# Kernel optimization log

Hardware: AMD Instinct MI355X
Metric: run time of the kernel (lower is better)

The kernel has to match this reference:

```python
import jax, jax.numpy as jnp
import numpy as np

NUM_WIRES = 14
N_LAYERS = 4
BATCH = 128


def _rx_mat(theta):
    # PennyLane RX(t) = [[cos(t/2), -i sin(t/2)], [-i sin(t/2), cos(t/2)]]
    c = jnp.cos(theta / 2).astype(jnp.complex64)
    s = jnp.sin(theta / 2).astype(jnp.complex64)
    row0 = jnp.stack([c, -1j * s], axis=-1)
    row1 = jnp.stack([-1j * s, c], axis=-1)
    return jnp.stack([row0, row1], axis=-2)  # (..., 2, 2)


def _rz_mat(theta):
    # PennyLane RZ(t) = diag(exp(-it/2), exp(it/2))
    e0 = jnp.exp(-1j * theta.astype(jnp.complex64) / 2)
    e1 = jnp.exp(1j * theta.astype(jnp.complex64) / 2)
    z = jnp.zeros_like(e0)
    row0 = jnp.stack([e0, z], axis=-1)
    row1 = jnp.stack([z, e1], axis=-1)
    return jnp.stack([row0, row1], axis=-2)


def _apply_1q(psi, gate, wire):
    # psi: (B, 2, 2, ..., 2); gate: (2,2) shared or (B,2,2) per-sample
    axis = wire + 1
    psi = jnp.moveaxis(psi, axis, -1)
    if gate.ndim == 2:
        psi = psi @ gate.T
    else:
        psi = jnp.einsum('b...j,bij->b...i', psi, gate)
    return jnp.moveaxis(psi, -1, axis)


def _apply_cnot(psi, ctrl, tgt):
    ac, at = ctrl + 1, tgt + 1
    psi0 = jnp.take(psi, 0, axis=ac)
    psi1 = jnp.take(psi, 1, axis=ac)
    at_adj = at - (1 if at > ac else 0)  # target axis shifts after removing ctrl axis
    psi1 = jnp.flip(psi1, axis=at_adj)   # X on target when ctrl=1
    return jnp.stack([psi0, psi1], axis=ac)


def _circuit(x, weights):
    # x: (B, n) real angles; weights: (L, n, 2)
    B = x.shape[0]
    n = NUM_WIRES
    psi = jnp.zeros((B,) + (2,) * n, jnp.complex64)
    psi = psi.at[(slice(None),) + (0,) * n].set(1.0)  # |0...0>
    # data encoding: per-sample RX gates
    for i in range(n):
        psi = _apply_1q(psi, _rx_mat(x[:, i]), i)
    # variational ansatz
    for l in range(N_LAYERS):
        for i in range(n):
            psi = _apply_1q(psi, _rx_mat(weights[l, i, 0]), i)
            psi = _apply_1q(psi, _rz_mat(weights[l, i, 1]), i)
        for i in range(n - 1):
            psi = _apply_cnot(psi, i, i + 1)
        psi = _apply_cnot(psi, n - 1, 0)
    # <Z_i> for every wire
    p = jnp.abs(psi) ** 2  # (B, 2, ..., 2) real
    zs = []
    for i in range(n):
        other = tuple(a for a in range(1, n + 1) if a != i + 1)
        m = jnp.sum(p, axis=other)  # (B, 2)
        zs.append(m[:, 0] - m[:, 1])
    return jnp.stack(zs, axis=-1)  # (B, n)


def setup_inputs() -> dict:
    key = jax.random.key(0)
    k1, k2, k3, k4 = jax.random.split(key, 4)
    states = jax.random.normal(k1, (BATCH, 2 ** NUM_WIRES), dtype=jnp.float32)
    weights = jax.random.normal(k2, (N_LAYERS, NUM_WIRES, 2), dtype=jnp.float32)
    lim = 1.0 / np.sqrt(NUM_WIRES)
    head_w = jax.random.uniform(k3, (1, NUM_WIRES), jnp.float32, -lim, lim)
    head_b = jax.random.uniform(k4, (1,), jnp.float32, -lim, lim)
    return {"states": states, "weights": weights, "head_w": head_w, "head_b": head_b}


def reference(states, weights, head_w, head_b):
    features = jnp.abs(states)[:, :NUM_WIRES]        # (B, n)
    qfeatures = _circuit(features, weights)          # (B, n)
    out = (qfeatures @ head_w.T + head_b)[:, 0]      # (B,)
    return out
```

## Files before the change

kernel.cpp:

```cpp
#include <hip/hip_runtime.h>
#include <math.h>

#define NW 14
#define NSTATE 16384
#define HALF 8192
#define NL 4
#define BATCH 128
#define TPB 1024
#define SHB1 (84 * 1024)
#define SHB2 ((NSTATE + 3 * TPB) * (int)sizeof(float2))


#define B12_ 0x3FFFu
#define B13_ 0x1FFFu

#define WAVE_FENCE() __builtin_amdgcn_wave_barrier()

__device__ __forceinline__ unsigned sxmap(unsigned v) {
    unsigned t = v;
    t ^= t >> 1; t ^= t >> 2; t ^= t >> 4; t ^= t >> 8;
    return (t & 0x0FFFu) | ((t & 1u) << 13);
}

__device__ __forceinline__ float2 cmul(float2 u, float2 v) {
    return make_float2(u.x * v.x - u.y * v.y, u.x * v.y + u.y * v.x);
}

__device__ __forceinline__ float4 fused_coef(const float* weights,
                                             const float* states,
                                             int b, int l, int w) {
    float t1 = weights[(l * NW + w) * 2 + 0];
    float t2 = weights[(l * NW + w) * 2 + 1];
    if (l == 0) t1 += fabsf(states[(size_t)b * NSTATE + w]);
    float s, c, sz, cz;
    sincosf(0.5f * t1, &s, &c);
    sincosf(0.5f * t2, &sz, &cz);
    return make_float4(c * cz, -c * sz, -s * sz, -s * cz);
}

template<int N, int M>
__device__ __forceinline__ void gateN(float2* r, float4 g, unsigned s3) {
    const float f = (s3 & (unsigned)M) ? -1.0f : 1.0f;
    g.y *= f;
    g.z *= f;
#pragma unroll
    for (int k = 0; k < N; ++k) {
        if ((k & M) == 0) {
            const float x0 = r[k].x,   y0 = r[k].y;
            const float x1 = r[k|M].x, y1 = r[k|M].y;
            r[k].x   =  g.x*x0 - g.y*y0 + g.z*x1 - g.w*y1;
            r[k].y   =  g.x*y0 + g.y*x0 + g.z*y1 + g.w*x1;
            r[k|M].x = -g.z*x0 - g.w*y0 + g.x*x1 + g.y*y1;
            r[k|M].y = -g.z*y0 + g.w*x0 + g.x*y1 - g.y*x1;
        }
    }
}

template<int J0, int S3SH, int S3MSK>
__device__ __forceinline__ void pass3h(float2* psi, const float4* gc,
                                       unsigned t) {
    const float4 gA = gc[13 - (J0 + 0)];
    const float4 gB = gc[13 - (J0 + 1)];
    const float4 gC = gc[13 - (J0 + 2)];
    const unsigned s3   = (t >> S3SH) & (unsigned)S3MSK;
    const unsigned low  = t & ((1u << J0) - 1u);
    const unsigned high = (t >> J0) << (J0 + 3);
    float2 r[8];
#pragma unroll
    for (int k = 0; k < 8; ++k)
        r[k] = psi[low | (((unsigned)k ^ s3) << J0) | high];
    gateN<8,1>(r, gA, s3);
    gateN<8,2>(r, gB, s3);
    gateN<8,4>(r, gC, s3);
#pragma unroll
    for (int k = 0; k < 8; ++k)
        psi[low | (((unsigned)k ^ s3) << J0) | high] = r[k];
}

template<int J0, bool SWZ>
__device__ __forceinline__ void pass4f(float2* psi, const float4* gc,
                                       unsigned t) {
    const float4 gA = gc[13 - (J0 + 0)];
    const float4 gB = gc[13 - (J0 + 1)];
    const float4 gC = gc[13 - (J0 + 2)];
    const float4 gD = gc[13 - (J0 + 3)];
    const unsigned s    = SWZ ? (t & 15u) : 0u;
    const unsigned low  = t & ((1u << J0) - 1u);
    const unsigned high = (t >> J0) << (J0 + 4);
    float2 r[16];
#pragma unroll
    for (int k = 0; k < 16; ++k)
        r[k] = psi[low | (((unsigned)k ^ s) << J0) | high];
    gateN<16,1>(r, gA, s);
    gateN<16,2>(r, gB, s);
    gateN<16,4>(r, gC, s);
    gateN<16,8>(r, gD, s);
#pragma unroll
    for (int k = 0; k < 16; ++k)
        psi[low | (((unsigned)k ^ s) << J0) | high] = r[k];
}

__device__ __forceinline__ void passE(float2* psi, float2* spare,
                                      const float4* gc4, int l, unsigned t) {
    const float4 g1 = gc4[l*NW + 1];
    const float4 g0 = gc4[l*NW + 0];

    unsigned v = t;
    v ^= v >> 1; v ^= v >> 2; v ^= v >> 4; v ^= v >> 8;
    const unsigned Rinv0 = (v & 0x0FFFu) | ((v & 1u) << 13);

    float2 c0[4];
#pragma unroll
    for (int k = 0; k < 4; ++k) c0[k] = psi[t | ((unsigned)k << 12)];
    gateN<4,1>(c0, g1, 0u);
    gateN<4,2>(c0, g0, 0u);
    spare[3*t+0] = c0[1];
    spare[3*t+1] = c0[2];
    spare[3*t+2] = c0[3];
    const float2 keep = c0[0];

    float2 r[12];
#pragma unroll
    for (int m = 1; m < 4; ++m) {
        const unsigned base = t | ((unsigned)m << 10);
#pragma unroll
        for (int k = 0; k < 4; ++k)
            r[(m-1)*4 + k] = psi[base | ((unsigned)k << 12)];
    }
#pragma unroll
    for (int m = 0; m < 3; ++m) {
        gateN<4,1>(r + 4*m, g1, 0u);
        gateN<4,2>(r + 4*m, g0, 0u);
    }

    __syncthreads();

#pragma unroll
    for (int m = 1; m < 4; ++m) {
        const unsigned Rb = Rinv0 ^ ((m & 1) ? 0x27FFu : 0u)
                                  ^ ((m & 2) ? 0x2FFFu : 0u);
#pragma unroll
        for (int k = 0; k < 4; ++k) {
            const unsigned CK = ((k & 1) ? B12_ : 0u) ^ ((k & 2) ? B13_ : 0u);
            psi[Rb ^ CK] = r[(m-1)*4 + k];
        }
    }
    psi[Rinv0]           = keep;
    psi[Rinv0 ^ B12_]    = spare[3*t+0];
    psi[Rinv0 ^ B13_]    = spare[3*t+1];
    psi[Rinv0 ^ 0x2000u] = spare[3*t+2];
}

__device__ __forceinline__ void exit_scatter(const float2* psi,
                                             float2* __restrict__ dst,
                                             float4 g1, unsigned q,
                                             unsigned tid) {
#pragma unroll
    for (int m = 0; m < 4; ++m) {
        const unsigned jc = tid + (unsigned)m * TPB;
        const float2 x0 = psi[jc];
        const float2 x1 = psi[jc | 0x1000u];
        float2 A0, A1;
        A0.x =  g1.x*x0.x - g1.y*x0.y + g1.z*x1.x - g1.w*x1.y;
        A0.y =  g1.x*x0.y + g1.y*x0.x + g1.z*x1.y + g1.w*x1.x;
        A1.x = -g1.z*x0.x - g1.w*x0.y + g1.x*x1.x + g1.y*x1.y;
        A1.y = -g1.z*x0.y + g1.w*x0.x + g1.x*x1.y - g1.y*x1.x;
        const unsigned d0 = sxmap(jc) ^ (q ? 0x1FFFu : 0u);
        dst[d0]           = A0;
        dst[d0 ^ 0x3FFFu] = A1;
    }
}

__global__ __launch_bounds__(TPB) void k_layer1(
    const float* __restrict__ states, const float* __restrict__ weights,
    float2* __restrict__ Sout)
{
    extern __shared__ float2 psi[];
    __shared__ float2 vfac[NW][2];
    __shared__ float2 T1[128];
    __shared__ float2 T2[128];
    __shared__ float4 gc[NW];
    const unsigned gid = blockIdx.x, q = gid >> 7, b = gid & 127u;
    const unsigned tid = threadIdx.x;

    if (tid < NW) {
        float4 g = fused_coef(weights, states, (int)b, 0, (int)tid);
        vfac[tid][0] = make_float2(g.x, g.y);
        vfac[tid][1] = make_float2(-g.z, g.w);
    }
    if (tid >= 64 && tid < 64 + NW)
        gc[tid - 64] = fused_coef(weights, states, (int)b, 1, (int)(tid - 64));
    __syncthreads();
    if (tid < 128) {
        float2 p = make_float2(1.0f, 0.0f);
#pragma unroll
        for (int j = 0; j < 7; ++j)
            p = cmul(p, vfac[13 - j][(tid >> j) & 1u]);
        T1[tid] = p;
    } else if (tid < 256) {
        const unsigned u = tid - 128;
        float2 p = make_float2(1.0f, 0.0f);
#pragma unroll
        for (int j = 7; j < 14; ++j)
            p = cmul(p, vfac[13 - j][(u >> (j - 7)) & 1u]);
        T2[u] = p;
    }
    __syncthreads();

#pragma unroll
    for (int m = 0; m < 8; ++m) {
        const unsigned I  = tid + (unsigned)m * TPB;
        const unsigned If = I | (q << 13);
        const unsigned lo  = (If ^ (If >> 1)) & 0x0FFFu;
        const unsigned y12 = ((If >> 12) ^ (If >> 13) ^ If) & 1u;
        const unsigned y13 = ((If >> 13) ^ If) & 1u;
        const unsigned J = lo | (y12 << 12) | (y13 << 13);
        psi[I] = cmul(T1[J & 127u], T2[J >> 7]);
    }
    __syncthreads();

    pass3h<0, 1, 7>(psi, gc, tid);  WAVE_FENCE();
    pass3h<3, 3, 1>(psi, gc, tid);  WAVE_FENCE();
    pass3h<6, 0, 0>(psi, gc, tid);  __syncthreads();
    pass3h<9, 0, 0>(psi, gc, tid);  __syncthreads();

    exit_scatter(psi, Sout + (size_t)b * NSTATE, gc[1], q, tid);
}

__global__ __launch_bounds__(TPB) void k_rest(
    const float* __restrict__ states, const float* __restrict__ weights,
    const float* __restrict__ head_w, const float* __restrict__ head_b,
    const float2* __restrict__ Sin, float* __restrict__ out)
{
    extern __shared__ float2 dyn[];
    float2* psi   = dyn;
    float2* spare = dyn + NSTATE;
    __shared__ float4 gc4[NL * NW];
    __shared__ float wsum[TPB / 64];
    const unsigned b = blockIdx.x;
    const unsigned tid = threadIdx.x;

    if (tid < NL * NW)
        gc4[tid] = fused_coef(weights, states, (int)b,
                              (int)tid / NW, (int)tid % NW);
    __syncthreads();

    {
        const float4 ge = gc4[1 * NW + 0];
#pragma unroll
        for (int qm = 0; qm < 8; ++qm) {
            const unsigned q = (unsigned)qm >> 2;
            const unsigned m = (unsigned)qm & 3u;
            const float2* src = Sin + (size_t)b * NSTATE + (size_t)q * HALF;
            const unsigned ic = tid + m * TPB;
            const float2 f0 = src[ic];
            const float2 f1 = src[ic ^ 0x1FFFu];
            const unsigned rc = (q ^ ic) & 1u;
            const float aar = ge.x, aai = rc ? -ge.y : ge.y;
            const float bbr = rc ? -ge.z : ge.z, bbi = ge.w;
            float2 oc, op;
            oc.x = aar*f0.x - aai*f0.y + bbr*f1.x - bbi*f1.y;
            oc.y = aar*f0.y + aai*f0.x + bbr*f1.y + bbi*f1.x;
            op.x = aar*f1.x + aai*f1.y - (bbr*f0.x + bbi*f0.y);
            op.y = aar*f1.y - aai*f1.x - (bbr*f0.y - bbi*f0.x);
            psi[(q << 13) | ic]            = oc;
            psi[(q << 13) | (ic ^ 0x1FFFu)] = op;
        }
    }
    __syncthreads();

    pass4f<0, true >(psi, gc4 + 2 * NW, tid);  WAVE_FENCE();
    pass4f<4, false>(psi, gc4 + 2 * NW, tid);  __syncthreads();
    pass4f<8, false>(psi, gc4 + 2 * NW, tid);  __syncthreads();
    passE(psi, spare, gc4, 2, tid);            __syncthreads();

    pass4f<0, true >(psi, gc4 + 3 * NW, tid);  WAVE_FENCE();
    pass4f<4, false>(psi, gc4 + 3 * NW, tid);  __syncthreads();
    pass4f<8, false>(psi, gc4 + 3 * NW, tid);  __syncthreads();

    float hw[NW];
#pragma unroll
    for (int i = 0; i < NW; ++i) hw[i] = head_w[i];
    float H = 0.0f, H12 = 0.0f;
#pragma unroll
    for (int i = 0; i < NW; ++i) H += hw[i];
#pragma unroll
    for (int i = 2; i < NW; ++i) H12 += hw[i];

    const float4 g1 = gc4[3 * NW + 1];
    const float4 g0 = gc4[3 * NW + 0];

    float acc = 0.0f;
#pragma unroll
    for (int m2 = 0; m2 < 4; ++m2) {
        const unsigned base = tid | ((unsigned)m2 << 10);
        float2 r[4];
#pragma unroll
        for (int k = 0; k < 4; ++k)
            r[k] = psi[base | ((unsigned)k << 12)];
        gateN<4,1>(r, g1, 0u);
        gateN<4,2>(r, g0, 0u);
        float A = 0.0f;
        unsigned sfx = 0u;
#pragma unroll
        for (int p = 11; p >= 0; --p) {
            sfx ^= (base >> p) & 1u;
            if (sfx) A += hw[13 - p];
        }
        const unsigned P = sfx;
#pragma unroll
        for (int k = 0; k < 4; ++k) {
            const unsigned u   = ((unsigned)k ^ ((unsigned)k >> 1)) & 1u;
            const unsigned b13 = P ^ ((unsigned)k & 1u);
            float sum = u ? (H12 - A) : A;
            if (u)   sum += hw[1];
            if (b13) sum += hw[0];
            const float cv = H - 2.0f * sum;
            acc += (r[k].x * r[k].x + r[k].y * r[k].y) * cv;
        }
    }
#pragma unroll
    for (int off = 32; off > 0; off >>= 1)
        acc += __shfl_down(acc, off, 64);
    if ((tid & 63u) == 0) wsum[tid >> 6] = acc;
    __syncthreads();
    if (tid == 0) {
        float tot = 0.0f;
#pragma unroll
        for (int i = 0; i < TPB / 64; ++i) tot += wsum[i];
        out[b] = tot + head_b[0];
    }
}

extern "C" void kernel_launch(void* const* d_in, const int* in_sizes, int n_in,
                              void* d_out, int out_size, void* d_ws, size_t ws_size,
                              hipStream_t stream) {
    const float* states  = (const float*)d_in[0];
    const float* weights = (const float*)d_in[1];
    const float* head_w  = (const float*)d_in[2];
    const float* head_b  = (const float*)d_in[3];
    float* out = (float*)d_out;

    float2* SA = (float2*)d_ws;

    k_layer1<<<2 * BATCH, TPB, SHB1, stream>>>(states, weights, SA);
    k_rest  <<<BATCH, TPB, SHB2, stream>>>(states, weights, head_w, head_b,
                                           SA, out);
}
```

Measured before the change: 102.2 us.

## Split layer 2 into its own half-state kernel across 256 blocks

Layer 2 of the ansatz moves out of the single-block-per-sample k_rest kernel into a new k_layer2 kernel. Like layer 1, k_layer2 splits each sample's state across two blocks (256 blocks in total) and writes an intermediate state to a second workspace buffer. The final kernel then handles only layer 3 and the readout. The aim is more parallelism, since 128 blocks underfill the GPU. The cost is an extra launch plus a full global-memory round trip of the state.

```diff
diff --git a/kernel.cpp b/kernel.cpp
--- a/kernel.cpp
+++ b/kernel.cpp
@@ -98,57 +98,6 @@
 #pragma unroll
     for (int k = 0; k < 16; ++k)
         psi[low | (((unsigned)k ^ s) << J0) | high] = r[k];
-}
-
-__device__ __forceinline__ void passE(float2* psi, float2* spare,
-                                      const float4* gc4, int l, unsigned t) {
-    const float4 g1 = gc4[l*NW + 1];
-    const float4 g0 = gc4[l*NW + 0];
-
-    unsigned v = t;
-    v ^= v >> 1; v ^= v >> 2; v ^= v >> 4; v ^= v >> 8;
-    const unsigned Rinv0 = (v & 0x0FFFu) | ((v & 1u) << 13);
-
-    float2 c0[4];
-#pragma unroll
-    for (int k = 0; k < 4; ++k) c0[k] = psi[t | ((unsigned)k << 12)];
-    gateN<4,1>(c0, g1, 0u);
-    gateN<4,2>(c0, g0, 0u);
-    spare[3*t+0] = c0[1];
-    spare[3*t+1] = c0[2];
-    spare[3*t+2] = c0[3];
-    const float2 keep = c0[0];
-
-    float2 r[12];
-#pragma unroll
-    for (int m = 1; m < 4; ++m) {
-        const unsigned base = t | ((unsigned)m << 10);
-#pragma unroll
-        for (int k = 0; k < 4; ++k)
-            r[(m-1)*4 + k] = psi[base | ((unsigned)k << 12)];
-    }
-#pragma unroll
-    for (int m = 0; m < 3; ++m) {
-        gateN<4,1>(r + 4*m, g1, 0u);
-        gateN<4,2>(r + 4*m, g0, 0u);
-    }
-
-    __syncthreads();
-
-#pragma unroll
-    for (int m = 1; m < 4; ++m) {
-        const unsigned Rb = Rinv0 ^ ((m & 1) ? 0x27FFu : 0u)
-                                  ^ ((m & 2) ? 0x2FFFu : 0u);
-#pragma unroll
-        for (int k = 0; k < 4; ++k) {
-            const unsigned CK = ((k & 1) ? B12_ : 0u) ^ ((k & 2) ? B13_ : 0u);
-            psi[Rb ^ CK] = r[(m-1)*4 + k];
-        }
-    }
-    psi[Rinv0]           = keep;
-    psi[Rinv0 ^ B12_]    = spare[3*t+0];
-    psi[Rinv0 ^ B13_]    = spare[3*t+1];
-    psi[Rinv0 ^ 0x2000u] = spare[3*t+2];
 }
 
 __device__ __forceinline__ void exit_scatter(const float2* psi,
@@ -171,6 +120,27 @@
     }
 }
 
+__device__ __forceinline__ void entry_gate(const float2* __restrict__ src,
+                                           float2* psi, float4 ge,
+                                           unsigned q, unsigned tid) {
+#pragma unroll
+    for (int m = 0; m < 4; ++m) {
+        const unsigned ic = tid + (unsigned)m * TPB;
+        const float2 f0 = src[ic];
+        const float2 f1 = src[ic ^ 0x1FFFu];
+        const unsigned rc = (q ^ ic) & 1u;
+        const float aar = ge.x, aai = rc ? -ge.y : ge.y;
+        const float bbr = rc ? -ge.z : ge.z, bbi = ge.w;
+        float2 oc, op;
+        oc.x = aar*f0.x - aai*f0.y + bbr*f1.x - bbi*f1.y;
+        oc.y = aar*f0.y + aai*f0.x + bbr*f1.y + bbi*f1.x;
+        op.x = aar*f1.x + aai*f1.y - (bbr*f0.x + bbi*f0.y);
+        op.y = aar*f1.y - aai*f1.x - (bbr*f0.y - bbi*f0.x);
+        psi[ic]           = oc;
+        psi[ic ^ 0x1FFFu] = op;
+    }
+}
+
 __global__ __launch_bounds__(TPB) void k_layer1(
     const float* __restrict__ states, const float* __restrict__ weights,
     float2* __restrict__ Sout)
@@ -227,26 +197,50 @@
     exit_scatter(psi, Sout + (size_t)b * NSTATE, gc[1], q, tid);
 }
 
-__global__ __launch_bounds__(TPB) void k_rest(
+__global__ __launch_bounds__(TPB) void k_layer2(
+    const float* __restrict__ states, const float* __restrict__ weights,
+    const float2* __restrict__ Sin, float2* __restrict__ Sout)
+{
+    extern __shared__ float2 psi[];
+    __shared__ float4 gc[NW];
+    __shared__ float4 ge_s;
+    const unsigned gid = blockIdx.x, q = gid >> 7, b = gid & 127u;
+    const unsigned tid = threadIdx.x;
+
+    if (tid < NW) gc[tid] = fused_coef(weights, states, (int)b, 2, (int)tid);
+    if (tid == NW) ge_s = fused_coef(weights, states, (int)b, 1, 0);
+    __syncthreads();
+
+    entry_gate(Sin + (size_t)b * NSTATE + (size_t)q * HALF, psi, ge_s, q, tid);
+    __syncthreads();
+
+    pass3h<0, 1, 7>(psi, gc, tid);  WAVE_FENCE();
+    pass3h<3, 3, 1>(psi, gc, tid);  WAVE_FENCE();
+    pass3h<6, 0, 0>(psi, gc, tid);  __syncthreads();
+    pass3h<9, 0, 0>(psi, gc, tid);  __syncthreads();
+
+    exit_scatter(psi, Sout + (size_t)b * NSTATE, gc[1], q, tid);
+}
+
+__global__ __launch_bounds__(TPB) void k_rest3(
     const float* __restrict__ states, const float* __restrict__ weights,
     const float* __restrict__ head_w, const float* __restrict__ head_b,
     const float2* __restrict__ Sin, float* __restrict__ out)
 {
     extern __shared__ float2 dyn[];
-    float2* psi   = dyn;
-    float2* spare = dyn + NSTATE;
-    __shared__ float4 gc4[NL * NW];
+    float2* psi = dyn;
+    __shared__ float4 gc3[NW];
+    __shared__ float4 ge_s;
     __shared__ float wsum[TPB / 64];
     const unsigned b = blockIdx.x;
     const unsigned tid = threadIdx.x;
 
-    if (tid < NL * NW)
-        gc4[tid] = fused_coef(weights, states, (int)b,
-                              (int)tid / NW, (int)tid % NW);
+    if (tid < NW) gc3[tid] = fused_coef(weights, states, (int)b, 3, (int)tid);
+    if (tid == NW) ge_s = fused_coef(weights, states, (int)b, 2, 0);
     __syncthreads();
 
     {
-        const float4 ge = gc4[1 * NW + 0];
+        const float4 ge = ge_s;
 #pragma unroll
         for (int qm = 0; qm < 8; ++qm) {
             const unsigned q = (unsigned)qm >> 2;
@@ -269,14 +263,9 @@
     }
     __syncthreads();
 
-    pass4f<0, true >(psi, gc4 + 2 * NW, tid);  WAVE_FENCE();
-    pass4f<4, false>(psi, gc4 + 2 * NW, tid);  __syncthreads();
-    pass4f<8, false>(psi, gc4 + 2 * NW, tid);  __syncthreads();
-    passE(psi, spare, gc4, 2, tid);            __syncthreads();
-
-    pass4f<0, true >(psi, gc4 + 3 * NW, tid);  WAVE_FENCE();
-    pass4f<4, false>(psi, gc4 + 3 * NW, tid);  __syncthreads();
-    pass4f<8, false>(psi, gc4 + 3 * NW, tid);  __syncthreads();
+    pass4f<0, true >(psi, gc3, tid);  WAVE_FENCE();
+    pass4f<4, false>(psi, gc3, tid);  __syncthreads();
+    pass4f<8, false>(psi, gc3, tid);  __syncthreads();
 
     float hw[NW];
 #pragma unroll
@@ -287,8 +276,8 @@
 #pragma unroll
     for (int i = 2; i < NW; ++i) H12 += hw[i];
 
-    const float4 g1 = gc4[3 * NW + 1];
-    const float4 g0 = gc4[3 * NW + 0];
+    const float4 g1 = gc3[1];
+    const float4 g0 = gc3[0];
 
     float acc = 0.0f;
 #pragma unroll
@@ -342,8 +331,10 @@
     float* out = (float*)d_out;
 
     float2* SA = (float2*)d_ws;
+    float2* SB = SA + (size_t)BATCH * NSTATE;
 
     k_layer1<<<2 * BATCH, TPB, SHB1, stream>>>(states, weights, SA);
-    k_rest  <<<BATCH, TPB, SHB2, stream>>>(states, weights, head_w, head_b,
-                                           SA, out);
-}
+    k_layer2<<<2 * BATCH, TPB, SHB1, stream>>>(states, weights, SA, SB);
+    k_rest3 <<<BATCH, TPB, SHB2, stream>>>(states, weights, head_w, head_b,
+                                           SB, out);
+}
```

After: 117.9 us. +15.3%, slower.
